# Optimization experiments

Hardware: AMD Instinct MI355X
Metric: run time of the kernel (lower is better)

## Reference

```python
import jax, jax.numpy as jnp
import numpy as np
from jax import lax

B, T, D, H, L = 512, 512, 32, 64, 2
ALPHA, BETA = 2.0 / 5.0, 4.0 / 5.0  # GRUFlowBlock contraction constants


def setup_inputs() -> dict:
    key = jax.random.key(0)
    ks = jax.random.split(key, 16)
    s = 1.0 / np.sqrt(H + 1)
    inp = {
        "x": jax.random.normal(ks[0], (B, T, D), jnp.float32),
        "t": jax.random.uniform(ks[1], (B, T, 1), jnp.float32),
        # GRU-flow layer params (spectral norm folded into weight values)
        "flow_W_hr": jax.random.normal(ks[2], (L, H, H + 1), jnp.float32) * s,
        "flow_b_hr": jax.random.normal(ks[3], (L, H), jnp.float32) * 0.01,
        "flow_W_hz": jax.random.normal(ks[4], (L, H, H + 1), jnp.float32) * s,
        "flow_b_hz": jax.random.normal(ks[5], (L, H), jnp.float32) * 0.01,
        "flow_W_hh": jax.random.normal(ks[6], (L, H, H + 1), jnp.float32) * s,
        "flow_b_hh": jax.random.normal(ks[7], (L, H), jnp.float32) * 0.01,
        # TimeTanh: tanh(w * t), per-dim scale w
        "flow_tw": jax.random.normal(ks[8], (L, H), jnp.float32),
        # nn.GRU(D, H) single layer, batch_first
        "gru_W_ih": jax.random.normal(ks[9], (3 * H, D), jnp.float32) / np.sqrt(H),
        "gru_W_hh": jax.random.normal(ks[10], (3 * H, H), jnp.float32) / np.sqrt(H),
        "gru_b_ih": jax.random.normal(ks[11], (3 * H,), jnp.float32) / np.sqrt(H),
        "gru_b_hh": jax.random.normal(ks[12], (3 * H,), jnp.float32) / np.sqrt(H),
    }
    return inp


def _flow(h, tt, flow_W_hr, flow_b_hr, flow_W_hz, flow_b_hz, flow_W_hh, flow_b_hh, flow_tw):
    # h: [B, H], tt: [B, 1]
    for l in range(L):
        inp = jnp.concatenate([h, tt], -1)  # [B, H+1]
        r = BETA * jax.nn.sigmoid(inp @ flow_W_hr[l].T + flow_b_hr[l])
        z = ALPHA * jax.nn.sigmoid(inp @ flow_W_hz[l].T + flow_b_hz[l])
        u = jnp.tanh(jnp.concatenate([r * h, tt], -1) @ flow_W_hh[l].T + flow_b_hh[l])
        h = h + jnp.tanh(flow_tw[l] * tt) * (z * (u - h))
    return h


def _gru_cell(xt, h, gru_W_ih, gru_W_hh, gru_b_ih, gru_b_hh):
    gi = xt @ gru_W_ih.T + gru_b_ih  # [B, 3H]
    gh = h @ gru_W_hh.T + gru_b_hh
    i_r, i_z, i_n = jnp.split(gi, 3, -1)
    h_r, h_z, h_n = jnp.split(gh, 3, -1)
    r = jax.nn.sigmoid(i_r + h_r)
    z = jax.nn.sigmoid(i_z + h_z)
    n = jnp.tanh(i_n + r * h_n)
    return (1.0 - z) * n + z * h


def reference(x, t, flow_W_hr, flow_b_hr, flow_W_hz, flow_b_hz, flow_W_hh, flow_b_hh,
              flow_tw, gru_W_ih, gru_W_hh, gru_b_ih, gru_b_hh):
    def step(h, xt_tt):
        xt, tt = xt_tt  # [B, D], [B, 1]
        h = _flow(h, tt, flow_W_hr, flow_b_hr, flow_W_hz, flow_b_hz,
                  flow_W_hh, flow_b_hh, flow_tw)
        h_out = h  # hiddens stores the post-flow, pre-GRU state
        h_new = _gru_cell(xt, h, gru_W_ih, gru_W_hh, gru_b_ih, gru_b_hh)
        return h_new, h_out

    h0 = jnp.zeros((x.shape[0], H), x.dtype)
    xs = (jnp.swapaxes(x, 0, 1), jnp.swapaxes(t, 0, 1))  # time-major for scan
    _, hiddens = lax.scan(step, h0, xs)  # [T, B, H]
    return jnp.swapaxes(hiddens, 0, 1)  # [B, T, H]
```

## Files before the change

### kernel.cpp

```cpp
#include <hip/hip_runtime.h>


#define NT 512
#define ND 32
#define NH 64
#define NL 2

__device__ __forceinline__ float sigm(float v) {
    return __builtin_amdgcn_rcpf(1.0f + __expf(-v));
}
__device__ __forceinline__ float tanh_(float v) {
    return 1.0f - 2.0f * __builtin_amdgcn_rcpf(1.0f + __expf(2.0f * v));
}
#define PIN(v) asm volatile("" : "+v"(v))

__global__ __launch_bounds__(512, 2) void cgru_fused(
    const float* __restrict__ x, const float* __restrict__ tin,
    const float* __restrict__ Whr, const float* __restrict__ bhr,
    const float* __restrict__ Whz, const float* __restrict__ bhz,
    const float* __restrict__ Whh, const float* __restrict__ bhh,
    const float* __restrict__ tw,
    const float* __restrict__ gWih, const float* __restrict__ gWhh,
    const float* __restrict__ gbih, const float* __restrict__ gbhh,
    float* __restrict__ out)
{
    const int tid = threadIdx.x;
    const int j   = tid >> 3;
    const int q   = tid & 7;
    const int qh  = q & 3;
    const bool isZ = q >= 4;
    const int b0  = blockIdx.x * 2;

    __shared__ float hS[2][NH];
    __shared__ float rhS[2][NH];
    __shared__ float hxS[2][128];

    const float* Wsrc = isZ ? Whz : Whr;
    const float* bsrc = isZ ? bhz : bhr;
    float wrz[NL][16], wu[NL][8];
    float w65rz[NL], w65u[NL], brz[NL], bu[NL], tws[NL];
#pragma unroll
    for (int l = 0; l < NL; ++l) {
        const int row = (l * NH + j) * (NH + 1);
#pragma unroll
        for (int k = 0; k < 16; ++k) wrz[l][k] = Wsrc[row + qh * 16 + k];
#pragma unroll
        for (int k = 0; k < 8; ++k)  wu[l][k]  = Whh[row + q * 8 + k];
        w65rz[l] = Wsrc[row + NH];
        w65u[l]  = Whh[row + NH];
        brz[l]   = bsrc[l * NH + j];
        bu[l]    = bhh[l * NH + j];
        tws[l]   = tw[l * NH + j];
    }

    const int grow = (isZ ? NH : 0) + j;
    float g1[24];
#pragma unroll
    for (int k = 0; k < 24; ++k) {
        const int m = qh * 24 + k;
        g1[k] = (m < NH) ? gWhh[grow * NH + m] : gWih[grow * ND + (m - NH)];
    }
    const float bg1 = gbih[grow] + gbhh[grow];

    float g2[16];
    if (!isZ) {
#pragma unroll
        for (int k = 0; k < 16; ++k) g2[k] = gWhh[(2 * NH + j) * NH + qh * 16 + k];
    } else {
#pragma unroll
        for (int k = 0; k < 8; ++k)  g2[k] = gWih[(2 * NH + j) * ND + qh * 8 + k];
#pragma unroll
        for (int k = 8; k < 16; ++k) g2[k] = 0.0f;
    }
    const float bin = gbih[2 * NH + j];
    const float bhn = gbhh[2 * NH + j];

#pragma unroll
    for (int l = 0; l < NL; ++l) {
#pragma unroll
        for (int k = 0; k < 16; ++k) PIN(wrz[l][k]);
#pragma unroll
        for (int k = 0; k < 8; ++k)  PIN(wu[l][k]);
        PIN(w65rz[l]); PIN(w65u[l]); PIN(brz[l]); PIN(bu[l]); PIN(tws[l]);
    }
#pragma unroll
    for (int k = 0; k < 24; ++k) PIN(g1[k]);
#pragma unroll
    for (int k = 0; k < 16; ++k) PIN(g2[k]);
    float bg1p = bg1, binp = bin, bhnp = bhn;
    PIN(bg1p); PIN(binp); PIN(bhnp);

    if (tid < 2 * NH) ((float*)hS)[tid] = 0.0f;
    if (tid < 2 * ND) hxS[tid >> 5][96 + (tid & 31)] = 0.0f;
    __syncthreads();

    const float* xptr = x + (size_t)(b0 + (tid >= ND ? 1 : 0)) * NT * ND;
    const float* tp0  = tin + (size_t)b0 * NT;
    const float* tp1  = tin + (size_t)(b0 + 1) * NT;
    float* op0 = out + (size_t)b0 * NT * NH;
    float* op1 = out + (size_t)(b0 + 1) * NT * NH;

    float xv = 0.0f;
    if (tid < 2 * ND) xv = xptr[tid & 31];
    float tt0 = tp0[0], tt1 = tp1[0];

    for (int ts = 0; ts < NT; ++ts) {
        float xnext = 0.0f, ttn0 = 0.0f, ttn1 = 0.0f;
        if (ts + 1 < NT) {
            if (tid < 2 * ND) xnext = xptr[(ts + 1) * ND + (tid & 31)];
            ttn0 = tp0[ts + 1];
            ttn1 = tp1[ts + 1];
        }

#pragma unroll
        for (int l = 0; l < NL; ++l) {
            float a0 = 0.0f, a1 = 0.0f;
            {
                const float* hp0 = &hS[0][qh * 16];
                const float* hp1 = &hS[1][qh * 16];
#pragma unroll
                for (int k = 0; k < 16; ++k) {
                    a0 = fmaf(wrz[l][k], hp0[k], a0);
                    a1 = fmaf(wrz[l][k], hp1[k], a1);
                }
            }
            a0 += __shfl_xor(a0, 1); a0 += __shfl_xor(a0, 2);
            a1 += __shfl_xor(a1, 1); a1 += __shfl_xor(a1, 2);
            const float s0 = sigm(a0 + w65rz[l] * tt0 + brz[l]);
            const float s1 = sigm(a1 + w65rz[l] * tt1 + brz[l]);
            const float zv0 = 0.4f * s0;
            const float zv1 = 0.4f * s1;
            if (q == 0) {
                rhS[0][j] = (0.8f * s0) * hS[0][j];
                rhS[1][j] = (0.8f * s1) * hS[1][j];
            }
            __syncthreads();

            float u0 = 0.0f, u1 = 0.0f;
            {
                const float* rp0 = &rhS[0][q * 8];
                const float* rp1 = &rhS[1][q * 8];
#pragma unroll
                for (int k = 0; k < 8; ++k) {
                    u0 = fmaf(wu[l][k], rp0[k], u0);
                    u1 = fmaf(wu[l][k], rp1[k], u1);
                }
            }
            u0 += __shfl_xor(u0, 1); u0 += __shfl_xor(u0, 2); u0 += __shfl_xor(u0, 4);
            u1 += __shfl_xor(u1, 1); u1 += __shfl_xor(u1, 2); u1 += __shfl_xor(u1, 4);
            if (l == NL - 1 && tid < 2 * ND)
                hxS[tid >> 5][NH + (tid & 31)] = xv;
            const float uu0 = tanh_(u0 + w65u[l] * tt0 + bu[l]);
            const float uu1 = tanh_(u1 + w65u[l] * tt1 + bu[l]);
            if (q == 4) {
                const float h0 = hS[0][j];
                const float h1 = hS[1][j];
                const float hn0 = fmaf(tanh_(tws[l] * tt0) * zv0, uu0 - h0, h0);
                const float hn1 = fmaf(tanh_(tws[l] * tt1) * zv1, uu1 - h1, h1);
                hS[0][j] = hn0;
                hS[1][j] = hn1;
                if (l == NL - 1) {
                    hxS[0][j] = hn0;
                    hxS[1][j] = hn1;
                    op0[ts * NH + j] = hn0;
                    op1[ts * NH + j] = hn1;
                }
            }
            __syncthreads();
        }

        float p0 = 0.0f, p1 = 0.0f;
        {
            const float* gp0 = &hxS[0][qh * 24];
            const float* gp1 = &hxS[1][qh * 24];
#pragma unroll
            for (int k = 0; k < 24; ++k) {
                p0 = fmaf(g1[k], gp0[k], p0);
                p1 = fmaf(g1[k], gp1[k], p1);
            }
        }
        p0 += __shfl_xor(p0, 1); p0 += __shfl_xor(p0, 2);
        p1 += __shfl_xor(p1, 1); p1 += __shfl_xor(p1, 2);
        const float gate0 = sigm(p0 + bg1p);
        const float gate1 = sigm(p1 + bg1p);
        const float oth0  = __shfl_xor(gate0, 4);
        const float oth1  = __shfl_xor(gate1, 4);
        const float r0 = isZ ? oth0 : gate0;
        const float r1 = isZ ? oth1 : gate1;
        const float z0 = isZ ? gate0 : oth0;
        const float z1 = isZ ? gate1 : oth1;

        float d0 = 0.0f, d1 = 0.0f;
        {
            const int off = isZ ? (NH + qh * 8) : (qh * 16);
            const float* dp0 = &hxS[0][off];
            const float* dp1 = &hxS[1][off];
#pragma unroll
            for (int k = 0; k < 16; ++k) {
                d0 = fmaf(g2[k], dp0[k], d0);
                d1 = fmaf(g2[k], dp1[k], d1);
            }
        }
        d0 += __shfl_xor(d0, 1); d0 += __shfl_xor(d0, 2);
        d1 += __shfl_xor(d1, 1); d1 += __shfl_xor(d1, 2);
        const float e0 = __shfl_xor(d0, 4);
        const float e1 = __shfl_xor(d1, 4);
        const float hnd0 = isZ ? e0 : d0;
        const float hnd1 = isZ ? e1 : d1;
        const float ind0 = isZ ? d0 : e0;
        const float ind1 = isZ ? d1 : e1;

        const float n0 = tanh_(ind0 + binp + r0 * (hnd0 + bhnp));
        const float n1 = tanh_(ind1 + binp + r1 * (hnd1 + bhnp));
        const float hj0 = hxS[0][j];
        const float hj1 = hxS[1][j];
        const float hp20 = (1.0f - z0) * n0 + z0 * hj0;
        const float hp21 = (1.0f - z1) * n1 + z1 * hj1;
        if (q == 0) {
            hS[0][j] = hp20;
            hS[1][j] = hp21;
        }
        __syncthreads();

        xv = xnext; tt0 = ttn0; tt1 = ttn1;
    }
}

extern "C" void kernel_launch(void* const* d_in, const int* in_sizes, int n_in,
                              void* d_out, int out_size, void* d_ws, size_t ws_size,
                              hipStream_t stream) {
    const float* x    = (const float*)d_in[0];
    const float* tin  = (const float*)d_in[1];
    const float* Whr  = (const float*)d_in[2];
    const float* bhr  = (const float*)d_in[3];
    const float* Whz  = (const float*)d_in[4];
    const float* bhz  = (const float*)d_in[5];
    const float* Whh  = (const float*)d_in[6];
    const float* bhh  = (const float*)d_in[7];
    const float* tw   = (const float*)d_in[8];
    const float* gWih = (const float*)d_in[9];
    const float* gWhh = (const float*)d_in[10];
    const float* gbih = (const float*)d_in[11];
    const float* gbhh = (const float*)d_in[12];
    float* out = (float*)d_out;

    dim3 grid(256), block(512);
    hipLaunchKernelGGL(cgru_fused, grid, block, 0, stream,
                       x, tin, Whr, bhr, Whz, bhz, Whh, bhh, tw,
                       gWih, gWhh, gbih, gbhh, out);
}
```

Baseline: 1.383 ms.

## Store recurrent weights as packed fp16 registers and use DPP reductions

A pre-kernel converts the flow and GRU weight matrices to fp16 in workspace. The fused kernel keeps those weights as half2 pairs in registers, which halves the register footprint, and requests 4 waves per EU to allow more occupancy. The first two butterfly reduction steps switch from shuffles to DPP adds, and the PIN asm barriers are removed. The cost is extra convert instructions per FMA, reduced weight precision, and an additional kernel launch.

Result: slower. 1.720 ms (+24.3%).

```diff
diff --git a/kernel.cpp b/kernel.cpp
--- a/kernel.cpp
+++ b/kernel.cpp
@@ -1,4 +1,5 @@
 #include <hip/hip_runtime.h>
+#include <hip/hip_fp16.h>
 
 
 #define NT 512
@@ -12,16 +13,42 @@
 __device__ __forceinline__ float tanh_(float v) {
     return 1.0f - 2.0f * __builtin_amdgcn_rcpf(1.0f + __expf(2.0f * v));
 }
-#define PIN(v) asm volatile("" : "+v"(v))
-
-__global__ __launch_bounds__(512, 2) void cgru_fused(
+__device__ __forceinline__ float dpp_add_xor1(float x) {
+    int y = __builtin_amdgcn_update_dpp(0, __float_as_int(x), 0xB1, 0xF, 0xF, true);
+    return x + __int_as_float(y);
+}
+__device__ __forceinline__ float dpp_add_xor2(float x) {
+    int y = __builtin_amdgcn_update_dpp(0, __float_as_int(x), 0x4E, 0xF, 0xF, true);
+    return x + __int_as_float(y);
+}
+
+__global__ __launch_bounds__(256) void cvt_weights(
+    const float* __restrict__ Whr, const float* __restrict__ Whz,
+    const float* __restrict__ Whh, const float* __restrict__ gWih,
+    const float* __restrict__ gWhh, __half* __restrict__ dst)
+{
+    const int i = blockIdx.x * 256 + threadIdx.x;
+    if (i < 24576) {
+        const int a = i >> 13, rem = i & 8191;
+        const int row = rem >> 6, c = rem & 63;
+        const float* src = (a == 0) ? Whr : ((a == 1) ? Whz : Whh);
+        dst[i] = __float2half(src[row * 65 + c]);
+    } else if (i < 30720) {
+        dst[i] = __float2half(gWih[i - 24576]);
+    } else if (i < 43008) {
+        dst[i] = __float2half(gWhh[i - 30720]);
+    }
+}
+
+__global__ __launch_bounds__(512) __attribute__((amdgpu_waves_per_eu(4, 4)))
+void cgru_fused(
     const float* __restrict__ x, const float* __restrict__ tin,
     const float* __restrict__ Whr, const float* __restrict__ bhr,
     const float* __restrict__ Whz, const float* __restrict__ bhz,
     const float* __restrict__ Whh, const float* __restrict__ bhh,
     const float* __restrict__ tw,
-    const float* __restrict__ gWih, const float* __restrict__ gWhh,
     const float* __restrict__ gbih, const float* __restrict__ gbhh,
+    const __half2* __restrict__ hw,
     float* __restrict__ out)
 {
     const int tid = threadIdx.x;
@@ -35,60 +62,53 @@
     __shared__ float rhS[2][NH];
     __shared__ float hxS[2][128];
 
-    const float* Wsrc = isZ ? Whz : Whr;
-    const float* bsrc = isZ ? bhz : bhr;
-    float wrz[NL][16], wu[NL][8];
+    const __half2* hWr = hw;
+    const __half2* hWz = hw + 4096;
+    const __half2* hWh = hw + 8192;
+    const __half2* hWi = hw + 12288;
+    const __half2* hWg = hw + 15360;
+
+    const __half2* Wsrc2 = isZ ? hWz : hWr;
+    const float*   Wsrcf = isZ ? Whz : Whr;
+    const float*   bsrc  = isZ ? bhz : bhr;
+    __half2 wrz2[NL][8], wu2[NL][4];
     float w65rz[NL], w65u[NL], brz[NL], bu[NL], tws[NL];
 #pragma unroll
     for (int l = 0; l < NL; ++l) {
-        const int row = (l * NH + j) * (NH + 1);
-#pragma unroll
-        for (int k = 0; k < 16; ++k) wrz[l][k] = Wsrc[row + qh * 16 + k];
-#pragma unroll
-        for (int k = 0; k < 8; ++k)  wu[l][k]  = Whh[row + q * 8 + k];
-        w65rz[l] = Wsrc[row + NH];
-        w65u[l]  = Whh[row + NH];
+        const int rowp = (l * NH + j) * 32;
+#pragma unroll
+        for (int k = 0; k < 8; ++k) wrz2[l][k] = Wsrc2[rowp + qh * 8 + k];
+#pragma unroll
+        for (int k = 0; k < 4; ++k) wu2[l][k]  = hWh[rowp + q * 4 + k];
+        const int rowf = (l * NH + j) * (NH + 1);
+        w65rz[l] = Wsrcf[rowf + NH];
+        w65u[l]  = Whh[rowf + NH];
         brz[l]   = bsrc[l * NH + j];
         bu[l]    = bhh[l * NH + j];
         tws[l]   = tw[l * NH + j];
     }
 
     const int grow = (isZ ? NH : 0) + j;
-    float g1[24];
-#pragma unroll
-    for (int k = 0; k < 24; ++k) {
-        const int m = qh * 24 + k;
-        g1[k] = (m < NH) ? gWhh[grow * NH + m] : gWih[grow * ND + (m - NH)];
+    __half2 g12[12];
+#pragma unroll
+    for (int k = 0; k < 12; ++k) {
+        const int m2 = qh * 12 + k;
+        g12[k] = (m2 < 32) ? hWg[grow * 32 + m2] : hWi[grow * 16 + (m2 - 32)];
     }
     const float bg1 = gbih[grow] + gbhh[grow];
 
-    float g2[16];
+    __half2 g22[8];
     if (!isZ) {
 #pragma unroll
-        for (int k = 0; k < 16; ++k) g2[k] = gWhh[(2 * NH + j) * NH + qh * 16 + k];
+        for (int k = 0; k < 8; ++k) g22[k] = hWg[(2 * NH + j) * 32 + qh * 8 + k];
     } else {
 #pragma unroll
-        for (int k = 0; k < 8; ++k)  g2[k] = gWih[(2 * NH + j) * ND + qh * 8 + k];
-#pragma unroll
-        for (int k = 8; k < 16; ++k) g2[k] = 0.0f;
+        for (int k = 0; k < 4; ++k) g22[k] = hWi[(2 * NH + j) * 16 + qh * 4 + k];
+#pragma unroll
+        for (int k = 4; k < 8; ++k) g22[k] = __floats2half2_rn(0.0f, 0.0f);
     }
     const float bin = gbih[2 * NH + j];
     const float bhn = gbhh[2 * NH + j];
-
-#pragma unroll
-    for (int l = 0; l < NL; ++l) {
-#pragma unroll
-        for (int k = 0; k < 16; ++k) PIN(wrz[l][k]);
-#pragma unroll
-        for (int k = 0; k < 8; ++k)  PIN(wu[l][k]);
-        PIN(w65rz[l]); PIN(w65u[l]); PIN(brz[l]); PIN(bu[l]); PIN(tws[l]);
-    }
-#pragma unroll
-    for (int k = 0; k < 24; ++k) PIN(g1[k]);
-#pragma unroll
-    for (int k = 0; k < 16; ++k) PIN(g2[k]);
-    float bg1p = bg1, binp = bin, bhnp = bhn;
-    PIN(bg1p); PIN(binp); PIN(bhnp);
 
     if (tid < 2 * NH) ((float*)hS)[tid] = 0.0f;
     if (tid < 2 * ND) hxS[tid >> 5][96 + (tid & 31)] = 0.0f;
@@ -119,17 +139,18 @@
                 const float* hp0 = &hS[0][qh * 16];
                 const float* hp1 = &hS[1][qh * 16];
 #pragma unroll
-                for (int k = 0; k < 16; ++k) {
-                    a0 = fmaf(wrz[l][k], hp0[k], a0);
-                    a1 = fmaf(wrz[l][k], hp1[k], a1);
+                for (int k = 0; k < 8; ++k) {
+                    const float wl = __low2float(wrz2[l][k]);
+                    const float wh = __high2float(wrz2[l][k]);
+                    a0 = fmaf(wl, hp0[2 * k], a0); a0 = fmaf(wh, hp0[2 * k + 1], a0);
+                    a1 = fmaf(wl, hp1[2 * k], a1); a1 = fmaf(wh, hp1[2 * k + 1], a1);
                 }
             }
-            a0 += __shfl_xor(a0, 1); a0 += __shfl_xor(a0, 2);
-            a1 += __shfl_xor(a1, 1); a1 += __shfl_xor(a1, 2);
+            a0 = dpp_add_xor1(a0); a0 = dpp_add_xor2(a0);
+            a1 = dpp_add_xor1(a1); a1 = dpp_add_xor2(a1);
             const float s0 = sigm(a0 + w65rz[l] * tt0 + brz[l]);
             const float s1 = sigm(a1 + w65rz[l] * tt1 + brz[l]);
-            const float zv0 = 0.4f * s0;
-            const float zv1 = 0.4f * s1;
+            const float zv0 = 0.4f * s0, zv1 = 0.4f * s1;
             if (q == 0) {
                 rhS[0][j] = (0.8f * s0) * hS[0][j];
                 rhS[1][j] = (0.8f * s1) * hS[1][j];
@@ -141,13 +162,15 @@
                 const float* rp0 = &rhS[0][q * 8];
                 const float* rp1 = &rhS[1][q * 8];
 #pragma unroll
-                for (int k = 0; k < 8; ++k) {
-                    u0 = fmaf(wu[l][k], rp0[k], u0);
-                    u1 = fmaf(wu[l][k], rp1[k], u1);
+                for (int k = 0; k < 4; ++k) {
+                    const float wl = __low2float(wu2[l][k]);
+                    const float wh = __high2float(wu2[l][k]);
+                    u0 = fmaf(wl, rp0[2 * k], u0); u0 = fmaf(wh, rp0[2 * k + 1], u0);
+                    u1 = fmaf(wl, rp1[2 * k], u1); u1 = fmaf(wh, rp1[2 * k + 1], u1);
                 }
             }
-            u0 += __shfl_xor(u0, 1); u0 += __shfl_xor(u0, 2); u0 += __shfl_xor(u0, 4);
-            u1 += __shfl_xor(u1, 1); u1 += __shfl_xor(u1, 2); u1 += __shfl_xor(u1, 4);
+            u0 = dpp_add_xor1(u0); u0 = dpp_add_xor2(u0); u0 += __shfl_xor(u0, 4);
+            u1 = dpp_add_xor1(u1); u1 = dpp_add_xor2(u1); u1 += __shfl_xor(u1, 4);
             if (l == NL - 1 && tid < 2 * ND)
                 hxS[tid >> 5][NH + (tid & 31)] = xv;
             const float uu0 = tanh_(u0 + w65u[l] * tt0 + bu[l]);
@@ -174,15 +197,17 @@
             const float* gp0 = &hxS[0][qh * 24];
             const float* gp1 = &hxS[1][qh * 24];
 #pragma unroll
-            for (int k = 0; k < 24; ++k) {
-                p0 = fmaf(g1[k], gp0[k], p0);
-                p1 = fmaf(g1[k], gp1[k], p1);
-            }
-        }
-        p0 += __shfl_xor(p0, 1); p0 += __shfl_xor(p0, 2);
-        p1 += __shfl_xor(p1, 1); p1 += __shfl_xor(p1, 2);
-        const float gate0 = sigm(p0 + bg1p);
-        const float gate1 = sigm(p1 + bg1p);
+            for (int k = 0; k < 12; ++k) {
+                const float wl = __low2float(g12[k]);
+                const float wh = __high2float(g12[k]);
+                p0 = fmaf(wl, gp0[2 * k], p0); p0 = fmaf(wh, gp0[2 * k + 1], p0);
+                p1 = fmaf(wl, gp1[2 * k], p1); p1 = fmaf(wh, gp1[2 * k + 1], p1);
+            }
+        }
+        p0 = dpp_add_xor1(p0); p0 = dpp_add_xor2(p0);
+        p1 = dpp_add_xor1(p1); p1 = dpp_add_xor2(p1);
+        const float gate0 = sigm(p0 + bg1);
+        const float gate1 = sigm(p1 + bg1);
         const float oth0  = __shfl_xor(gate0, 4);
         const float oth1  = __shfl_xor(gate1, 4);
         const float r0 = isZ ? oth0 : gate0;
@@ -196,13 +221,15 @@
             const float* dp0 = &hxS[0][off];
             const float* dp1 = &hxS[1][off];
 #pragma unroll
-            for (int k = 0; k < 16; ++k) {
-                d0 = fmaf(g2[k], dp0[k], d0);
-                d1 = fmaf(g2[k], dp1[k], d1);
-            }
-        }
-        d0 += __shfl_xor(d0, 1); d0 += __shfl_xor(d0, 2);
-        d1 += __shfl_xor(d1, 1); d1 += __shfl_xor(d1, 2);
+            for (int k = 0; k < 8; ++k) {
+                const float wl = __low2float(g22[k]);
+                const float wh = __high2float(g22[k]);
+                d0 = fmaf(wl, dp0[2 * k], d0); d0 = fmaf(wh, dp0[2 * k + 1], d0);
+                d1 = fmaf(wl, dp1[2 * k], d1); d1 = fmaf(wh, dp1[2 * k + 1], d1);
+            }
+        }
+        d0 = dpp_add_xor1(d0); d0 = dpp_add_xor2(d0);
+        d1 = dpp_add_xor1(d1); d1 = dpp_add_xor2(d1);
         const float e0 = __shfl_xor(d0, 4);
         const float e1 = __shfl_xor(d1, 4);
         const float hnd0 = isZ ? e0 : d0;
@@ -210,8 +237,8 @@
         const float ind0 = isZ ? d0 : e0;
         const float ind1 = isZ ? d1 : e1;
 
-        const float n0 = tanh_(ind0 + binp + r0 * (hnd0 + bhnp));
-        const float n1 = tanh_(ind1 + binp + r1 * (hnd1 + bhnp));
+        const float n0 = tanh_(ind0 + bin + r0 * (hnd0 + bhn));
+        const float n1 = tanh_(ind1 + bin + r1 * (hnd1 + bhn));
         const float hj0 = hxS[0][j];
         const float hj1 = hxS[1][j];
         const float hp20 = (1.0f - z0) * n0 + z0 * hj0;
@@ -243,9 +270,11 @@
     const float* gbih = (const float*)d_in[11];
     const float* gbhh = (const float*)d_in[12];
     float* out = (float*)d_out;
-
-    dim3 grid(256), block(512);
-    hipLaunchKernelGGL(cgru_fused, grid, block, 0, stream,
+    __half* hws = (__half*)d_ws;
+
+    hipLaunchKernelGGL(cvt_weights, dim3(168), dim3(256), 0, stream,
+                       Whr, Whz, Whh, gWih, gWhh, hws);
+    hipLaunchKernelGGL(cgru_fused, dim3(256), dim3(512), 0, stream,
                        x, tin, Whr, bhr, Whz, bhz, Whh, bhh, tw,
-                       gWih, gWhh, gbih, gbhh, out);
-}
+                       gbih, gbhh, (const __half2*)hws, out);
+}
```
